# Kernel tuning notes

Hardware: AMD Instinct MI355X
Metric: run time of the kernel (lower is better)

The kernel has to match this reference:

```python
import jax, jax.numpy as jnp
import numpy as np

VAR_CENTER = 0.1   # variances[0]
VAR_SIZE = 0.2     # variances[1]
IOU_THRESHOLD = 0.5

B, T, P = 16, 64, 100000


def setup_inputs() -> dict:
    key = jax.random.key(0)
    kpc, kps, kc, ks, kl = jax.random.split(key, 5)
    # Priors in (cx, cy, w, h), relative coords in [0,1]
    p_cxcy = jax.random.uniform(kpc, (P, 2), dtype=jnp.float32) * 0.9 + 0.05
    p_wh = jax.random.uniform(kps, (P, 2), dtype=jnp.float32) * 0.15 + 0.02
    priors_xywha = jnp.concatenate([p_cxcy, p_wh], axis=-1)
    # Ground-truth boxes in xyxy (valid: x2>x1, y2>y1)
    centers = jax.random.uniform(kc, (B, T, 2), dtype=jnp.float32) * 0.8 + 0.1
    sizes = jax.random.uniform(ks, (B, T, 2), dtype=jnp.float32) * 0.15 + 0.02
    gt_boxes = jnp.concatenate([centers - sizes / 2, centers + sizes / 2], axis=-1)
    gt_labels = jax.random.randint(kl, (B, T), 1, 81, dtype=jnp.int32)
    return {"priors_xywha": priors_xywha, "gt_boxes": gt_boxes, "gt_labels": gt_labels}


def _box_iou(boxes1, boxes2):
    # boxes1: [T,4] xyxy, boxes2: [P,4] xyxy -> [T,P]
    area1 = (boxes1[:, 2] - boxes1[:, 0]) * (boxes1[:, 3] - boxes1[:, 1])  # [T]
    area2 = (boxes2[:, 2] - boxes2[:, 0]) * (boxes2[:, 3] - boxes2[:, 1])  # [P]
    lt = jnp.maximum(boxes1[:, None, :2], boxes2[None, :, :2])  # [T,P,2]
    rb = jnp.minimum(boxes1[:, None, 2:], boxes2[None, :, 2:])  # [T,P,2]
    wh = jnp.clip(rb - lt, 0.0)
    inter = wh[..., 0] * wh[..., 1]  # [T,P]
    return inter / (area1[:, None] + area2[None, :] - inter)


def reference(priors_xywha, gt_boxes, gt_labels):
    p_cxcy = priors_xywha[:, :2]
    p_wh = priors_xywha[:, 2:]
    priors_xyxy = jnp.concatenate([p_cxcy - p_wh / 2, p_cxcy + p_wh / 2], axis=-1)

    def per_image(boxes, labels):
        # boxes [T,4], labels [T]
        iou = _box_iou(boxes, priors_xyxy)            # [T,P]
        matched_vals = jnp.max(iou, axis=0)           # [P] best IoU per prior
        matches = jnp.argmax(iou, axis=0)             # [P] target index per prior
        best_prior = jnp.argmax(iou, axis=1)          # [T] best prior per target
        matches = matches.at[best_prior].set(jnp.arange(T))
        matched_vals = matched_vals.at[best_prior].set(2.0)
        lbl = labels[matches]                         # [P] irregular gather
        lbl = jnp.where(matched_vals < IOU_THRESHOLD, 0, lbl)
        mboxes = boxes[matches]                       # [P,4]
        b_cxcy = (mboxes[:, :2] + mboxes[:, 2:]) / 2
        b_wh = mboxes[:, 2:] - mboxes[:, :2]
        g_cxcy = (b_cxcy - p_cxcy) / (VAR_CENTER * p_wh)
        g_wh = jnp.log(b_wh / p_wh) / VAR_SIZE
        loc = jnp.concatenate([g_cxcy, g_wh], axis=-1)  # [P,4]
        return loc, lbl

    gt_locations, out_labels = jax.vmap(per_image)(gt_boxes, gt_labels)
    return gt_locations, out_labels
```

## Files before the change

### kernel.cpp

```cpp
#include <hip/hip_runtime.h>

#define T_GT 64
#define KP 4
#define TPB 256
#define NB 64

typedef unsigned int u32;
typedef unsigned long long u64;

__global__ void __launch_bounds__(256)
match_main(const float4* __restrict__ priors,
           const float4* __restrict__ gt_boxes,
           const int* __restrict__ gt_labels,
           u64* __restrict__ part,
           float* __restrict__ out_loc,
           float* __restrict__ out_lbl,
           int P, int NG) {
    __shared__ float4 s_gt[T_GT];
    __shared__ float  s_ga[T_GT];
    __shared__ int    s_lbl[T_GT];
    __shared__ u64    s_best[4][T_GT];
    __shared__ u64    s_tab[4][NB];

    const int tid  = threadIdx.x;
    const int lane = tid & 63;
    const int wv   = tid >> 6;
    const int b    = blockIdx.y;
    const int pbase = blockIdx.x * (TPB * KP);

    if (tid < T_GT) {
        const float4 gb = gt_boxes[b * T_GT + tid];
        s_gt[tid]  = gb;
        s_ga[tid]  = __fmul_rn(__fsub_rn(gb.z, gb.x), __fsub_rn(gb.w, gb.y));
        s_lbl[tid] = gt_labels[b * T_GT + tid];
    }
    s_best[wv][lane] = (u64)0xFFFFFFFFu;
    __syncthreads();

    {
        const float thL = (float)lane * (1.0f / NB);
        const float thR = thL + (1.0f / NB);
        u64 m = 0;
        if (wv == 0) {
            #pragma unroll 8
            for (int t = T_GT - 1; t >= 0; --t)
                m = m + m + ((s_gt[t].z > thL) ? 1u : 0u);
        } else if (wv == 1) {
            #pragma unroll 8
            for (int t = T_GT - 1; t >= 0; --t)
                m = m + m + ((s_gt[t].x < thR) ? 1u : 0u);
        } else if (wv == 2) {
            #pragma unroll 8
            for (int t = T_GT - 1; t >= 0; --t)
                m = m + m + ((s_gt[t].w > thL) ? 1u : 0u);
        } else {
            #pragma unroll 8
            for (int t = T_GT - 1; t >= 0; --t)
                m = m + m + ((s_gt[t].y < thR) ? 1u : 0u);
        }
        s_tab[wv][lane] = m;
    }
    __syncthreads();

    #pragma unroll
    for (int k = 0; k < KP; ++k) {
        const int p = pbase + k * TPB + tid;
        if (p < P) {
            const float4 pr = priors[p];
            const float px0 = __fsub_rn(pr.x, __fmul_rn(0.5f, pr.z));
            const float py0 = __fsub_rn(pr.y, __fmul_rn(0.5f, pr.w));
            const float px1 = __fadd_rn(pr.x, __fmul_rn(0.5f, pr.z));
            const float py1 = __fadd_rn(pr.y, __fmul_rn(0.5f, pr.w));
            const float pa  = __fmul_rn(__fsub_rn(px1, px0),
                                        __fsub_rn(py1, py0));

            const int bx0 = min(max(__float2int_rd(px0 * (float)NB), 0), NB - 1);
            const int bx1 = min(max(__float2int_rd(px1 * (float)NB), 0), NB - 1);
            const int by0 = min(max(__float2int_rd(py0 * (float)NB), 0), NB - 1);
            const int by1 = min(max(__float2int_rd(py1 * (float)NB), 0), NB - 1);

            u64 mask = s_tab[0][bx0] & s_tab[1][bx1] &
                       s_tab[2][by0] & s_tab[3][by1];

            u64 mbest = 63u;
            while (mask) {
                const int t = (int)__builtin_ctzll(mask);
                mask &= mask - 1;
                const float4 gb  = s_gt[t];
                const float  gar = s_ga[t];
                const float ltx = fmaxf(gb.x, px0);
                const float lty = fmaxf(gb.y, py0);
                const float rbx = fminf(gb.z, px1);
                const float rby = fminf(gb.w, py1);
                const float wx = fmaxf(__fsub_rn(rbx, ltx), 0.0f);
                const float wy = fmaxf(__fsub_rn(rby, lty), 0.0f);
                const float inter = __fmul_rn(wx, wy);
                const float uni = __fsub_rn(__fadd_rn(gar, pa), inter);
                const float q = __fdiv_rn(inter, uni);
                const u64 qh = (u64)__float_as_uint(q) << 32;
                const u64 mp = qh | (u32)(63 - t);
                if (mp > mbest) mbest = mp;
                atomicMax(&s_best[wv][t], qh | (u64)(0xFFFFFFFFu - (u32)p));
            }

            const int   t_best = 63 - (int)(mbest & 63u);
            const float q_best = __uint_as_float((u32)(mbest >> 32));
            const int   lbl = (q_best < 0.5f) ? 0 : s_lbl[t_best];

            const float4 mb = s_gt[t_best];
            const float  bcx = (mb.x + mb.z) * 0.5f;
            const float  bcy = (mb.y + mb.w) * 0.5f;
            const float  bw  = mb.z - mb.x;
            const float  bh  = mb.w - mb.y;

            const float lx = __fdividef(bcx - pr.x, 0.1f * pr.z);
            const float ly = __fdividef(bcy - pr.y, 0.1f * pr.w);
            const float lz = __logf(__fdividef(bw, pr.z)) * 5.0f;
            const float lw = __logf(__fdividef(bh, pr.w)) * 5.0f;

            float4* rowp = (float4*)(out_loc + ((size_t)b * P + p) * 4);
            *rowp = make_float4(lx, ly, lz, lw);
            out_lbl[(size_t)b * P + p] = (float)lbl;
        }
    }

    __syncthreads();
    if (tid < T_GT) {
        u64 m = s_best[0][tid];
        #pragma unroll
        for (int w = 1; w < 4; ++w) {
            const u64 v = s_best[w][tid];
            if (v > m) m = v;
        }
        part[((size_t)b * NG + blockIdx.x) * T_GT + tid] = m;
    }
}

__global__ void __launch_bounds__(256)
match_fin(const float4* __restrict__ priors,
          const float4* __restrict__ gt_boxes,
          const int* __restrict__ gt_labels,
          const u64* __restrict__ part,
          float* __restrict__ out_loc,
          float* __restrict__ out_lbl,
          int P, int NG) {
    __shared__ float4 s_gt[T_GT];
    __shared__ int    s_lbl[T_GT];
    __shared__ u64    s_best[4][T_GT];
    __shared__ u32    s_p[T_GT];

    const int tid = threadIdx.x;
    const int b   = blockIdx.x;
    const int t   = tid & 63;
    const int w   = tid >> 6;

    if (tid < T_GT) {
        s_gt[tid]  = gt_boxes[b * T_GT + tid];
        s_lbl[tid] = gt_labels[b * T_GT + tid];
    }

    const size_t base = (size_t)b * NG * T_GT + t;
    u64 m = 0;
    int g = w;
    for (; g + 12 < NG; g += 16) {
        const u64 a0 = part[base + (size_t)g * T_GT];
        const u64 a1 = part[base + (size_t)(g + 4) * T_GT];
        const u64 a2 = part[base + (size_t)(g + 8) * T_GT];
        const u64 a3 = part[base + (size_t)(g + 12) * T_GT];
        u64 x = a0 > a1 ? a0 : a1;
        const u64 y = a2 > a3 ? a2 : a3;
        if (y > x) x = y;
        if (x > m) m = x;
    }
    for (; g < NG; g += 4) {
        const u64 v = part[base + (size_t)g * T_GT];
        if (v > m) m = v;
    }
    s_best[w][t] = m;
    __syncthreads();
    if (tid < T_GT) {
        m = s_best[0][t];
        #pragma unroll
        for (int i = 1; i < 4; ++i) {
            const u64 v = s_best[i][t];
            if (v > m) m = v;
        }
        s_p[t] = 0xFFFFFFFFu - (u32)(m & 0xFFFFFFFFull);
    }
    __syncthreads();
    if (tid >= T_GT) return;

    const u32 p = s_p[tid];
    for (int u = tid + 1; u < T_GT; ++u)
        if (s_p[u] == p) return;

    const float4 pr = priors[p];
    const float4 mb = s_gt[tid];
    const float  bcx = (mb.x + mb.z) * 0.5f;
    const float  bcy = (mb.y + mb.w) * 0.5f;
    const float  bw  = mb.z - mb.x;
    const float  bh  = mb.w - mb.y;

    const float lx = __fdividef(bcx - pr.x, 0.1f * pr.z);
    const float ly = __fdividef(bcy - pr.y, 0.1f * pr.w);
    const float lz = __logf(__fdividef(bw, pr.z)) * 5.0f;
    const float lw = __logf(__fdividef(bh, pr.w)) * 5.0f;

    float4* rowp = (float4*)(out_loc + ((size_t)b * P + p) * 4);
    *rowp = make_float4(lx, ly, lz, lw);
    out_lbl[(size_t)b * P + p] = (float)s_lbl[tid];
}

extern "C" void kernel_launch(void* const* d_in, const int* in_sizes, int n_in,
                              void* d_out, int out_size, void* d_ws, size_t ws_size,
                              hipStream_t stream) {
    const float4* priors    = (const float4*)d_in[0];
    const float4* gt_boxes  = (const float4*)d_in[1];
    const int*    gt_labels = (const int*)d_in[2];

    const int P = in_sizes[0] / 4;
    const int B = in_sizes[2] / T_GT;

    float* out_loc = (float*)d_out;
    float* out_lbl = out_loc + (size_t)B * P * 4;

    const int NG = (P + TPB * KP - 1) / (TPB * KP);
    u64* part = (u64*)d_ws;

    dim3 g(NG, B);
    match_main<<<g, TPB, 0, stream>>>(priors, gt_boxes, gt_labels, part,
                                      out_loc, out_lbl, P, NG);
    match_fin<<<dim3(B), TPB, 0, stream>>>(priors, gt_boxes, gt_labels, part,
                                           out_loc, out_lbl, P, NG);
}
```

Measured before the change: 101.1 us.

## Build bin masks with ballots, keep GT boxes in registers via shuffles, refine bins

Each wavefront lane now holds one ground-truth box in registers. The per-bin overlap bitmasks are built with wave ballots instead of serial loops over shared memory, and the grid resolution doubles to 128 bins. Candidate boxes are fetched with cross-lane shuffles, with the whole wave iterating until every lane's mask is empty. Non-overlapping candidates skip the divide and the atomic. This cuts shared memory traffic and the number of false candidates, but lanes now sit idle while the lane with the most candidates finishes, and table building costs 128 ballots per wave.

```diff
diff --git a/kernel.cpp b/kernel.cpp
--- a/kernel.cpp
+++ b/kernel.cpp
@@ -3,7 +3,7 @@
 #define T_GT 64
 #define KP 4
 #define TPB 256
-#define NB 64
+#define NB 128
 
 typedef unsigned int u32;
 typedef unsigned long long u64;
@@ -16,11 +16,8 @@
            float* __restrict__ out_loc,
            float* __restrict__ out_lbl,
            int P, int NG) {
-    __shared__ float4 s_gt[T_GT];
-    __shared__ float  s_ga[T_GT];
-    __shared__ int    s_lbl[T_GT];
-    __shared__ u64    s_best[4][T_GT];
-    __shared__ u64    s_tab[4][NB];
+    __shared__ u64 s_best[4][T_GT];
+    __shared__ u64 s_tab[4][NB];
 
     const int tid  = threadIdx.x;
     const int lane = tid & 63;
@@ -28,96 +25,105 @@
     const int b    = blockIdx.y;
     const int pbase = blockIdx.x * (TPB * KP);
 
-    if (tid < T_GT) {
-        const float4 gb = gt_boxes[b * T_GT + tid];
-        s_gt[tid]  = gb;
-        s_ga[tid]  = __fmul_rn(__fsub_rn(gb.z, gb.x), __fsub_rn(gb.w, gb.y));
-        s_lbl[tid] = gt_labels[b * T_GT + tid];
-    }
+    const float4 gb  = gt_boxes[b * T_GT + lane];
+    const int    g_lb = gt_labels[b * T_GT + lane];
+
     s_best[wv][lane] = (u64)0xFFFFFFFFu;
-    __syncthreads();
-
-    {
-        const float thL = (float)lane * (1.0f / NB);
-        const float thR = thL + (1.0f / NB);
-        u64 m = 0;
-        if (wv == 0) {
-            #pragma unroll 8
-            for (int t = T_GT - 1; t >= 0; --t)
-                m = m + m + ((s_gt[t].z > thL) ? 1u : 0u);
-        } else if (wv == 1) {
-            #pragma unroll 8
-            for (int t = T_GT - 1; t >= 0; --t)
-                m = m + m + ((s_gt[t].x < thR) ? 1u : 0u);
-        } else if (wv == 2) {
-            #pragma unroll 8
-            for (int t = T_GT - 1; t >= 0; --t)
-                m = m + m + ((s_gt[t].w > thL) ? 1u : 0u);
-        } else {
-            #pragma unroll 8
-            for (int t = T_GT - 1; t >= 0; --t)
-                m = m + m + ((s_gt[t].y < thR) ? 1u : 0u);
-        }
-        s_tab[wv][lane] = m;
+
+    if (wv == 0) {
+        #pragma unroll 8
+        for (int bin = 0; bin < NB; ++bin) {
+            const u64 m = __ballot(gb.z > (float)bin * (1.0f / NB));
+            if (lane == 0) s_tab[0][bin] = m;
+        }
+    } else if (wv == 1) {
+        #pragma unroll 8
+        for (int bin = 0; bin < NB; ++bin) {
+            const u64 m = __ballot(gb.x < (float)(bin + 1) * (1.0f / NB));
+            if (lane == 0) s_tab[1][bin] = m;
+        }
+    } else if (wv == 2) {
+        #pragma unroll 8
+        for (int bin = 0; bin < NB; ++bin) {
+            const u64 m = __ballot(gb.w > (float)bin * (1.0f / NB));
+            if (lane == 0) s_tab[2][bin] = m;
+        }
+    } else {
+        #pragma unroll 8
+        for (int bin = 0; bin < NB; ++bin) {
+            const u64 m = __ballot(gb.y < (float)(bin + 1) * (1.0f / NB));
+            if (lane == 0) s_tab[3][bin] = m;
+        }
     }
     __syncthreads();
 
     #pragma unroll
     for (int k = 0; k < KP; ++k) {
-        const int p = pbase + k * TPB + tid;
-        if (p < P) {
-            const float4 pr = priors[p];
-            const float px0 = __fsub_rn(pr.x, __fmul_rn(0.5f, pr.z));
-            const float py0 = __fsub_rn(pr.y, __fmul_rn(0.5f, pr.w));
-            const float px1 = __fadd_rn(pr.x, __fmul_rn(0.5f, pr.z));
-            const float py1 = __fadd_rn(pr.y, __fmul_rn(0.5f, pr.w));
-            const float pa  = __fmul_rn(__fsub_rn(px1, px0),
-                                        __fsub_rn(py1, py0));
-
-            const int bx0 = min(max(__float2int_rd(px0 * (float)NB), 0), NB - 1);
-            const int bx1 = min(max(__float2int_rd(px1 * (float)NB), 0), NB - 1);
-            const int by0 = min(max(__float2int_rd(py0 * (float)NB), 0), NB - 1);
-            const int by1 = min(max(__float2int_rd(py1 * (float)NB), 0), NB - 1);
-
-            u64 mask = s_tab[0][bx0] & s_tab[1][bx1] &
-                       s_tab[2][by0] & s_tab[3][by1];
-
-            u64 mbest = 63u;
-            while (mask) {
-                const int t = (int)__builtin_ctzll(mask);
-                mask &= mask - 1;
-                const float4 gb  = s_gt[t];
-                const float  gar = s_ga[t];
-                const float ltx = fmaxf(gb.x, px0);
-                const float lty = fmaxf(gb.y, py0);
-                const float rbx = fminf(gb.z, px1);
-                const float rby = fminf(gb.w, py1);
-                const float wx = fmaxf(__fsub_rn(rbx, ltx), 0.0f);
-                const float wy = fmaxf(__fsub_rn(rby, lty), 0.0f);
-                const float inter = __fmul_rn(wx, wy);
+        const int p  = pbase + k * TPB + tid;
+        const int pe = min(p, P - 1);
+
+        const float4 pr = priors[pe];
+        const float px0 = __fsub_rn(pr.x, __fmul_rn(0.5f, pr.z));
+        const float py0 = __fsub_rn(pr.y, __fmul_rn(0.5f, pr.w));
+        const float px1 = __fadd_rn(pr.x, __fmul_rn(0.5f, pr.z));
+        const float py1 = __fadd_rn(pr.y, __fmul_rn(0.5f, pr.w));
+        const float pa  = __fmul_rn(__fsub_rn(px1, px0), __fsub_rn(py1, py0));
+
+        const int bx0 = min(max(__float2int_rd(px0 * (float)NB), 0), NB - 1);
+        const int bx1 = min(max(__float2int_rd(px1 * (float)NB), 0), NB - 1);
+        const int by0 = min(max(__float2int_rd(py0 * (float)NB), 0), NB - 1);
+        const int by1 = min(max(__float2int_rd(py1 * (float)NB), 0), NB - 1);
+
+        u64 mask = s_tab[0][bx0] & s_tab[1][bx1] &
+                   s_tab[2][by0] & s_tab[3][by1];
+
+        u64 mbest = 63u;
+        while (__any(mask != 0)) {
+            const bool live = (mask != 0);
+            const int  t = live ? (int)__builtin_ctzll(mask) : 0;
+            mask &= mask - 1;
+            const float gx0 = __shfl(gb.x, t, 64);
+            const float gy0 = __shfl(gb.y, t, 64);
+            const float gx1 = __shfl(gb.z, t, 64);
+            const float gy1 = __shfl(gb.w, t, 64);
+            const float gar = __fmul_rn(__fsub_rn(gx1, gx0),
+                                        __fsub_rn(gy1, gy0));
+
+            const float wx = fmaxf(__fsub_rn(fminf(gx1, px1),
+                                             fmaxf(gx0, px0)), 0.0f);
+            const float wy = fmaxf(__fsub_rn(fminf(gy1, py1),
+                                             fmaxf(gy0, py0)), 0.0f);
+            const float inter = __fmul_rn(wx, wy);
+            if (live && inter > 0.0f) {
                 const float uni = __fsub_rn(__fadd_rn(gar, pa), inter);
                 const float q = __fdiv_rn(inter, uni);
                 const u64 qh = (u64)__float_as_uint(q) << 32;
                 const u64 mp = qh | (u32)(63 - t);
                 if (mp > mbest) mbest = mp;
-                atomicMax(&s_best[wv][t], qh | (u64)(0xFFFFFFFFu - (u32)p));
+                atomicMax(&s_best[wv][t], qh | (u64)(0xFFFFFFFFu - (u32)pe));
             }
-
-            const int   t_best = 63 - (int)(mbest & 63u);
-            const float q_best = __uint_as_float((u32)(mbest >> 32));
-            const int   lbl = (q_best < 0.5f) ? 0 : s_lbl[t_best];
-
-            const float4 mb = s_gt[t_best];
-            const float  bcx = (mb.x + mb.z) * 0.5f;
-            const float  bcy = (mb.y + mb.w) * 0.5f;
-            const float  bw  = mb.z - mb.x;
-            const float  bh  = mb.w - mb.y;
-
-            const float lx = __fdividef(bcx - pr.x, 0.1f * pr.z);
-            const float ly = __fdividef(bcy - pr.y, 0.1f * pr.w);
-            const float lz = __logf(__fdividef(bw, pr.z)) * 5.0f;
-            const float lw = __logf(__fdividef(bh, pr.w)) * 5.0f;
-
+        }
+
+        const int   t_best = 63 - (int)(mbest & 63u);
+        const float q_best = __uint_as_float((u32)(mbest >> 32));
+        const float mx0 = __shfl(gb.x, t_best, 64);
+        const float my0 = __shfl(gb.y, t_best, 64);
+        const float mx1 = __shfl(gb.z, t_best, 64);
+        const float my1 = __shfl(gb.w, t_best, 64);
+        const int   tl  = __shfl(g_lb, t_best, 64);
+        const int   lbl = (q_best < 0.5f) ? 0 : tl;
+
+        const float bcx = (mx0 + mx1) * 0.5f;
+        const float bcy = (my0 + my1) * 0.5f;
+        const float bw  = mx1 - mx0;
+        const float bh  = my1 - my0;
+
+        const float lx = __fdividef(bcx - pr.x, 0.1f * pr.z);
+        const float ly = __fdividef(bcy - pr.y, 0.1f * pr.w);
+        const float lz = __logf(__fdividef(bw, pr.z)) * 5.0f;
+        const float lw = __logf(__fdividef(bh, pr.w)) * 5.0f;
+
+        if (p < P) {
             float4* rowp = (float4*)(out_loc + ((size_t)b * P + p) * 4);
             *rowp = make_float4(lx, ly, lz, lw);
             out_lbl[(size_t)b * P + p] = (float)lbl;
```

Measured after the change: 110.8 us. +9.6%, slower.
